# Performance work log

Measured on AMD Instinct MI355X. Metric: run time of the kernel, lower is better.

Reference implementation:

```python
import jax, jax.numpy as jnp
import numpy as np

N_USER, N_BADGE, E = 200_000, 50_000, 5_000_000
NEG_SLOPE = 0.2


def _gat(x_src, x_dst, src, dst, Ws, Wd, a_s, a_d, b, n_dst):
    """Bipartite single-head PyG GATConv (add_self_loops=False)."""
    hs = x_src @ Ws                      # [Ns, C]
    hd = x_dst @ Wd                      # [Nd, C]
    alpha_s = hs @ a_s                   # [Ns]
    alpha_d = hd @ a_d                   # [Nd]
    e = jax.nn.leaky_relu(alpha_s[src] + alpha_d[dst], NEG_SLOPE)  # [E]
    m = jax.ops.segment_max(e, dst, num_segments=n_dst)            # per-dst max
    w = jnp.exp(e - m[dst])
    s = jax.ops.segment_sum(w, dst, num_segments=n_dst) + 1e-16
    alpha = w / s[dst]                   # softmax over incoming edges
    out = jax.ops.segment_sum(alpha[:, None] * hs[src], dst, num_segments=n_dst)
    return out + b


def setup_inputs() -> dict:
    key = jax.random.key(0)
    ks = jax.random.split(key, 40)
    i = [0]
    def nk():
        k = ks[i[0]]; i[0] += 1; return k
    def nrm(shape, scale):
        return jax.random.normal(nk(), shape, jnp.float32) * scale
    inp = {
        "x_user": nrm((N_USER, 64), 1.0),
        "x_badge": nrm((N_BADGE, 64), 1.0),
        "ub_src": jax.random.randint(nk(), (E,), 0, N_USER, jnp.int32),
        "ub_dst": jax.random.randint(nk(), (E,), 0, N_BADGE, jnp.int32),
        "bu_src": jax.random.randint(nk(), (E,), 0, N_BADGE, jnp.int32),
        "bu_dst": jax.random.randint(nk(), (E,), 0, N_USER, jnp.int32),
        "ew_ub": jax.random.uniform(nk(), (E,), jnp.float32),
        "ew_bu": jax.random.uniform(nk(), (E,), jnp.float32),
    }
    s64, s16 = 1.0 / 8.0, 1.0 / 4.0  # ~glorot-ish scales for fan_in 64 / 16
    for rel in ("ub", "bu"):
        inp[f"W1_{rel}_s"] = nrm((64, 16), s64)
        inp[f"W1_{rel}_d"] = nrm((64, 16), s64)
        inp[f"a1_{rel}_s"] = nrm((16,), s16)
        inp[f"a1_{rel}_d"] = nrm((16,), s16)
        inp[f"b1_{rel}"] = jnp.zeros((16,), jnp.float32)
        inp[f"W2_{rel}_s"] = nrm((16, 2), s16)
        inp[f"W2_{rel}_d"] = nrm((16, 2), s16)
        inp[f"a2_{rel}_s"] = nrm((2,), 0.5)
        inp[f"a2_{rel}_d"] = nrm((2,), 0.5)
        inp[f"b2_{rel}"] = jnp.zeros((2,), jnp.float32)
    return inp


def reference(x_user, x_badge, ub_src, ub_dst, bu_src, bu_dst, ew_ub, ew_bu,
              W1_ub_s, W1_ub_d, a1_ub_s, a1_ub_d, b1_ub,
              W1_bu_s, W1_bu_d, a1_bu_s, a1_bu_d, b1_bu,
              W2_ub_s, W2_ub_d, a2_ub_s, a2_ub_d, b2_ub,
              W2_bu_s, W2_bu_d, a2_bu_s, a2_bu_d, b2_bu):
    # layer 1 (edge weights ignored: GATConv has edge_dim=None -> lin_edge is None)
    hb = _gat(x_user, x_badge, ub_src, ub_dst, W1_ub_s, W1_ub_d, a1_ub_s, a1_ub_d, b1_ub, N_BADGE)
    hu = _gat(x_badge, x_user, bu_src, bu_dst, W1_bu_s, W1_bu_d, a1_bu_s, a1_bu_d, b1_bu, N_USER)
    hu = jax.nn.relu(hu)
    hb = jax.nn.relu(hb)
    # layer 2
    ob = _gat(hu, hb, ub_src, ub_dst, W2_ub_s, W2_ub_d, a2_ub_s, a2_ub_d, b2_ub, N_BADGE)
    ou = _gat(hb, hu, bu_src, bu_dst, W2_bu_s, W2_bu_d, a2_bu_s, a2_bu_d, b2_bu, N_USER)
    return (ou, ob)
```

## Files before the change

kernel.cpp:

```cpp
#include <hip/hip_runtime.h>
#include <hip/hip_fp16.h>
#include <math.h>


#define NEG_SLOPE 0.2f
#define PART_PER 9760
#define NBC 196
#define CAPC 27072
#define NHALF 392
#define CAPH 13824
#define SHARD_DIV 50000

__device__ __forceinline__ float lrelu(float x) { return x > 0.f ? x : NEG_SLOPE * x; }

__global__ void k_stageA(
    const int* __restrict__ src0, const int* __restrict__ dst0,
    const int* __restrict__ src1, const int* __restrict__ dst1,
    int nE, int pblocks, unsigned* __restrict__ part0, unsigned* __restrict__ part1,
    int* __restrict__ bcnt,
    const float* __restrict__ xu, const float* __restrict__ xb,
    const float* __restrict__ Wub_s, const float* __restrict__ aub_s,
    const float* __restrict__ Wbu_d, const float* __restrict__ abu_d,
    const float* __restrict__ Wbu_s, const float* __restrict__ abu_s,
    const float* __restrict__ Wub_d, const float* __restrict__ aub_d,
    __half* __restrict__ hs_u, float* __restrict__ as_u, float* __restrict__ ad_u,
    __half* __restrict__ hs_b, float* __restrict__ as_b, float* __restrict__ ad_b,
    int NU, int NB, int gNU, int partBlocks, int nodeBlocks) {
  union Sm {
    struct { unsigned s_sorted[PART_PER]; int h[257]; int ps[256]; int resb[256]; int cur[256]; } p;
    struct { float sW[64 * 16]; float sa[16]; float sv[64]; } n;
  };
  __shared__ Sm sm;
  int t = threadIdx.x;
  int b = blockIdx.x;
  int k = min(nodeBlocks, partBlocks / 2);
  int inter = 3 * k;
  int partIdx = -1, nodeIdx = -1;
  if (b < inter) {
    if ((b % 3) == 2) nodeIdx = b / 3;
    else partIdx = (b / 3) * 2 + (b % 3);
  } else {
    int rem = b - inter;
    int ptail = partBlocks - 2 * k;
    if (rem < ptail) partIdx = 2 * k + rem;
    else nodeIdx = k + (rem - ptail);
  }
  if (partIdx >= 0) {
    int gb = partIdx;
    const int* src; const int* dst; unsigned* part; int* bc; int shift; int mask;
    if (gb < pblocks) { src = src0; dst = dst0; part = part0; bc = bcnt; shift = 8; mask = 255; }
    else { gb -= pblocks; src = src1; dst = dst1; part = part1; bc = bcnt + 256; shift = 10; mask = 1023; }
    int per = (nE + pblocks - 1) / pblocks;
    int beg = gb * per;
    int end = min(beg + per, nE);
    int cnt = end - beg;
    int cnt4 = cnt & ~3;
    sm.p.h[t] = 0;
    __syncthreads();
    for (int i = beg + t * 4; i + 3 < end; i += 1024) {
      int4 d4 = *(const int4*)(dst + i);
      atomicAdd(&sm.p.h[d4.x >> shift], 1);
      atomicAdd(&sm.p.h[d4.y >> shift], 1);
      atomicAdd(&sm.p.h[d4.z >> shift], 1);
      atomicAdd(&sm.p.h[d4.w >> shift], 1);
    }
    for (int i = beg + cnt4 + t; i < end; i += 256) atomicAdd(&sm.p.h[dst[i] >> shift], 1);
    __syncthreads();
    int v = sm.p.h[t];
    sm.p.ps[t] = v;
    __syncthreads();
    for (int off = 1; off < 256; off <<= 1) {
      int u = (t >= off) ? sm.p.ps[t - off] : 0;
      __syncthreads();
      sm.p.ps[t] += u;
      __syncthreads();
    }
    int excl = sm.p.ps[t] - v;
    sm.p.resb[t] = (t < NBC && v > 0) ? atomicAdd(&bc[t], v) : 0;
    __syncthreads();
    sm.p.h[t] = excl;
    sm.p.cur[t] = excl;
    if (t == 255) sm.p.h[256] = excl + v;
    __syncthreads();
    for (int i = beg + t * 4; i + 3 < end; i += 1024) {
      int4 d4 = *(const int4*)(dst + i);
      int4 s4 = *(const int4*)(src + i);
      int r;
      r = atomicAdd(&sm.p.cur[d4.x >> shift], 1);
      sm.p.s_sorted[r] = ((unsigned)(d4.x & mask) << 18) | (unsigned)s4.x;
      r = atomicAdd(&sm.p.cur[d4.y >> shift], 1);
      sm.p.s_sorted[r] = ((unsigned)(d4.y & mask) << 18) | (unsigned)s4.y;
      r = atomicAdd(&sm.p.cur[d4.z >> shift], 1);
      sm.p.s_sorted[r] = ((unsigned)(d4.z & mask) << 18) | (unsigned)s4.z;
      r = atomicAdd(&sm.p.cur[d4.w >> shift], 1);
      sm.p.s_sorted[r] = ((unsigned)(d4.w & mask) << 18) | (unsigned)s4.w;
    }
    for (int i = beg + cnt4 + t; i < end; i += 256) {
      int d = dst[i];
      int r = atomicAdd(&sm.p.cur[d >> shift], 1);
      sm.p.s_sorted[r] = ((unsigned)(d & mask) << 18) | (unsigned)src[i];
    }
    __syncthreads();
    for (int i = t; i < cnt; i += 1024) {
      int i1 = i + 256, i2 = i + 512, i3 = i + 768;
      int lo0 = 0, lo1 = 0, lo2 = 0, lo3 = 0;
      int hi0 = 256, hi1 = 256, hi2 = 256, hi3 = 256;
#pragma unroll
      for (int s = 0; s < 8; ++s) {
        int m0 = (lo0 + hi0) >> 1; if (sm.p.h[m0] <= i)  lo0 = m0; else hi0 = m0;
        int m1 = (lo1 + hi1) >> 1; if (sm.p.h[m1] <= i1) lo1 = m1; else hi1 = m1;
        int m2 = (lo2 + hi2) >> 1; if (sm.p.h[m2] <= i2) lo2 = m2; else hi2 = m2;
        int m3 = (lo3 + hi3) >> 1; if (sm.p.h[m3] <= i3) lo3 = m3; else hi3 = m3;
      }
      { int p = sm.p.resb[lo0] + (i - sm.p.h[lo0]);
        if (p < CAPC) part[(size_t)lo0 * CAPC + p] = sm.p.s_sorted[i]; }
      if (i1 < cnt) { int p = sm.p.resb[lo1] + (i1 - sm.p.h[lo1]);
        if (p < CAPC) part[(size_t)lo1 * CAPC + p] = sm.p.s_sorted[i1]; }
      if (i2 < cnt) { int p = sm.p.resb[lo2] + (i2 - sm.p.h[lo2]);
        if (p < CAPC) part[(size_t)lo2 * CAPC + p] = sm.p.s_sorted[i2]; }
      if (i3 < cnt) { int p = sm.p.resb[lo3] + (i3 - sm.p.h[lo3]);
        if (p < CAPC) part[(size_t)lo3 * CAPC + p] = sm.p.s_sorted[i3]; }
    }
    return;
  }
  int blk = nodeIdx;
  bool us = blk < gNU;
  const float* x  = us ? xu : xb;
  const float* Ws = us ? Wub_s : Wbu_s;
  const float* As = us ? aub_s : abu_s;
  const float* Wd = us ? Wbu_d : Wub_d;
  const float* Ad = us ? abu_d : aub_d;
  __half* hs = us ? hs_u : hs_b;
  float* als = us ? as_u : as_b;
  float* ald = us ? ad_u : ad_b;
  int N = us ? NU : NB;
  for (int i = t; i < 64 * 16; i += 256) sm.n.sW[i] = Ws[i];
  if (t < 16) sm.n.sa[t] = As[t];
  if (t < 64) {
    float s = 0.f;
    for (int c = 0; c < 16; ++c) s += Wd[t * 16 + c] * Ad[c];
    sm.n.sv[t] = s;
  }
  __syncthreads();
  int n = (us ? blk : blk - gNU) * 256 + t;
  if (n >= N) return;
  float acc[16];
#pragma unroll
  for (int c = 0; c < 16; ++c) acc[c] = 0.f;
  float ad = 0.f;
  const float4* xr4 = (const float4*)(x + (size_t)n * 64);
#pragma unroll 4
  for (int f4 = 0; f4 < 16; ++f4) {
    float4 xv4 = xr4[f4];
    float xv[4] = {xv4.x, xv4.y, xv4.z, xv4.w};
#pragma unroll
    for (int q = 0; q < 4; ++q) {
      int f = f4 * 4 + q;
#pragma unroll
      for (int c = 0; c < 16; ++c) acc[c] += xv[q] * sm.n.sW[f * 16 + c];
      ad += xv[q] * sm.n.sv[f];
    }
  }
  float al = 0.f;
#pragma unroll
  for (int c = 0; c < 16; ++c) {
    hs[(size_t)n * 16 + c] = __float2half(acc[c]);
    al += acc[c] * sm.n.sa[c];
  }
  als[n] = al;
  ald[n] = ad;
}

__global__ void k_sort2_both(const unsigned* __restrict__ part0,
                             const unsigned* __restrict__ part1,
                             const int* __restrict__ bcnt,
                             int* __restrict__ col0, int* __restrict__ col1,
                             int* __restrict__ rp0, int* __restrict__ rp1) {
  __shared__ unsigned s_sorted[CAPH];
  __shared__ int hist[512];
  __shared__ int ps[512];
  __shared__ int cur[512];
  __shared__ int s_tot;
  int bb = blockIdx.x;
  const unsigned* part; const int* bc; int* col; int* rp;
  int hsh, hmask, ns, sdiv;
  if (bb < NHALF) { part = part0; bc = bcnt; col = col0; rp = rp0;
                    hsh = 7; hmask = 127; ns = 4; sdiv = SHARD_DIV; }
  else { bb -= NHALF; part = part1; bc = bcnt + 256; col = col1; rp = rp1;
         hsh = 9; hmask = 511; ns = 1; sdiv = 1 << 30; }
  int t = threadIdx.x;
  int f = bb >> 1;
  int half = bb & 1;
  int cnt = min(bc[f], CAPC);
  int cnt4 = cnt & ~3;
  int slot = bb * CAPH;
  const unsigned* pp = part + (size_t)f * CAPC;
  hist[t] = 0;
  __syncthreads();
  for (int i = t * 4; i + 3 < cnt; i += 2048) {
    uint4 e4 = *(const uint4*)(pp + i);
    unsigned ee[4] = {e4.x, e4.y, e4.z, e4.w};
#pragma unroll
    for (int q = 0; q < 4; ++q) {
      int dl = (int)(ee[q] >> 18);
      if ((dl >> hsh) == half) {
        int sv = (int)(ee[q] & 0x3FFFFu);
        int bin = (ns == 4) ? ((dl & hmask) << 2) + sv / sdiv : (dl & hmask);
        atomicAdd(&hist[bin], 1);
      }
    }
  }
  for (int i = cnt4 + t; i < cnt; i += 512) {
    unsigned e = pp[i];
    int dl = (int)(e >> 18);
    if ((dl >> hsh) == half) {
      int sv = (int)(e & 0x3FFFFu);
      int bin = (ns == 4) ? ((dl & hmask) << 2) + sv / sdiv : (dl & hmask);
      atomicAdd(&hist[bin], 1);
    }
  }
  __syncthreads();
  int v = hist[t];
  ps[t] = v;
  __syncthreads();
  for (int off = 1; off < 512; off <<= 1) {
    int u = (t >= off) ? ps[t - off] : 0;
    __syncthreads();
    ps[t] += u;
    __syncthreads();
  }
  int excl = ps[t] - v;
  rp[bb * 513 + t] = slot + excl;
  if (t == 511) {
    int tot = min(ps[511], CAPH);
    rp[bb * 513 + 512] = slot + tot;
    s_tot = tot;
  }
  cur[t] = excl;
  __syncthreads();
  for (int i = t * 4; i + 3 < cnt; i += 2048) {
    uint4 e4 = *(const uint4*)(pp + i);
    unsigned ee[4] = {e4.x, e4.y, e4.z, e4.w};
#pragma unroll
    for (int q = 0; q < 4; ++q) {
      int dl = (int)(ee[q] >> 18);
      if ((dl >> hsh) == half) {
        int sv = (int)(ee[q] & 0x3FFFFu);
        int bin = (ns == 4) ? ((dl & hmask) << 2) + sv / sdiv : (dl & hmask);
        int r = atomicAdd(&cur[bin], 1);
        if (r < CAPH) s_sorted[r] = (unsigned)sv;
      }
    }
  }
  for (int i = cnt4 + t; i < cnt; i += 512) {
    unsigned e = pp[i];
    int dl = (int)(e >> 18);
    if ((dl >> hsh) == half) {
      int sv = (int)(e & 0x3FFFFu);
      int bin = (ns == 4) ? ((dl & hmask) << 2) + sv / sdiv : (dl & hmask);
      int r = atomicAdd(&cur[bin], 1);
      if (r < CAPH) s_sorted[r] = (unsigned)sv;
    }
  }
  __syncthreads();
  int tot = s_tot;
  for (int i = t; i < tot; i += 512) col[slot + i] = (int)s_sorted[i];
}

__device__ __forceinline__ void gat_pair8(
    const int* __restrict__ col, const __half* __restrict__ hs,
    int beg, int end, int j, float adv, const float (&sa)[8],
    float (&acc)[8], float& se) {
  int h = j & 1;
  int k0 = beg + (j >> 1);
  if (k0 >= end) return;
  int sv0 = col[k0];
  int k1 = k0 + 4;
  int sv1 = (k1 < end) ? col[k1] : -1;
  uint4 hv0 = *(const uint4*)(hs + (size_t)sv0 * 16 + h * 8);
  for (;;) {
    uint4 hv1 = hv0;
    int sv2 = -1;
    int k2 = k1 + 4;
    if (sv1 >= 0) {
      hv1 = *(const uint4*)(hs + (size_t)sv1 * 16 + h * 8);
      sv2 = (k2 < end) ? col[k2] : -1;
    }
    union { uint4 v; __half hh[8]; } b;
    b.v = hv0;
    float f[8];
    float p = 0.f;
#pragma unroll
    for (int cc = 0; cc < 8; ++cc) {
      f[cc] = __half2float(b.hh[cc]);
      p += f[cc] * sa[cc];
    }
    float afull = p + __shfl_xor(p, 1, 8);
    float w = __expf(lrelu(afull + adv));
    se += w;
#pragma unroll
    for (int cc = 0; cc < 8; ++cc) acc[cc] += w * f[cc];
    if (sv1 < 0) break;
    hv0 = hv1;
    sv1 = sv2;
    k1 = k2;
  }
}

__global__ void k_megaL1(
    const int* __restrict__ rp_ub, const int* __restrict__ col_ub,
    const float* __restrict__ a1s_ub, const float* __restrict__ ad_b,
    const __half* __restrict__ hs_u,
    float* __restrict__ acc_sl, float* __restrict__ se_sl,
    const int* __restrict__ rp_bu, const int* __restrict__ col_bu,
    const float* __restrict__ a1s_bu, const float* __restrict__ ad_u,
    const __half* __restrict__ hs_b,
    const float* __restrict__ b1bu,
    const float* __restrict__ W2ub_s, const float* __restrict__ a2ub_s,
    const float* __restrict__ W2bu_d, const float* __restrict__ a2bu_d,
    float4* __restrict__ pk_u, int NB, int NU, int ubBlocks) {
  __shared__ float sW2[32], sa2[2], sv2[16], sb1[16], sAub[16], sAbu[16];
  int t = threadIdx.x;
  if (t < 32) sW2[t] = W2ub_s[t];
  if (t < 2) sa2[t] = a2ub_s[t];
  if (t < 16) {
    float s = 0.f;
    for (int cc = 0; cc < 2; ++cc) s += W2bu_d[t * 2 + cc] * a2bu_d[cc];
    sv2[t] = s;
    sb1[t] = b1bu[t];
    sAub[t] = a1s_ub[t];
    sAbu[t] = a1s_bu[t];
  }
  __syncthreads();
  int b = blockIdx.x;
  int j = t & 7;
  int h = j & 1;
  if (b < ubBlocks) {
    int xcd = b & 7;
    int s = xcd >> 1;
    int sub = ((b >> 3) << 1) | (xcd & 1);
    int n = sub * 32 + (t >> 3);
    if (n >= NB) return;
    int base = (n >> 7) * 513 + (n & 127) * 4 + s;
    int beg = rp_ub[base], end = rp_ub[base + 1];
    float adv = ad_b[n];
    float sa[8];
#pragma unroll
    for (int cc = 0; cc < 8; ++cc) sa[cc] = sAub[h * 8 + cc];
    float acc[8];
#pragma unroll
    for (int cc = 0; cc < 8; ++cc) acc[cc] = 0.f;
    float se = 0.f;
    gat_pair8(col_ub, hs_u, beg, end, j, adv, sa, acc, se);
#pragma unroll
    for (int m = 2; m < 8; m <<= 1) {
      se += __shfl_xor(se, m, 8);
#pragma unroll
      for (int cc = 0; cc < 8; ++cc) acc[cc] += __shfl_xor(acc[cc], m, 8);
    }
    if (j < 2) {
      float* o = acc_sl + ((size_t)s * NB + n) * 16 + h * 8;
#pragma unroll
      for (int cc = 0; cc < 8; ++cc) o[cc] = acc[cc];
      if (j == 0) se_sl[s * NB + n] = se;
    }
  } else {
    int n = (b - ubBlocks) * 32 + (t >> 3);
    if (n >= NU) return;
    int base = (n >> 9) * 513 + (n & 511);
    int beg = rp_bu[base], end = rp_bu[base + 1];
    float adv = ad_u[n];
    float sa[8];
#pragma unroll
    for (int cc = 0; cc < 8; ++cc) sa[cc] = sAbu[h * 8 + cc];
    float acc[8];
#pragma unroll
    for (int cc = 0; cc < 8; ++cc) acc[cc] = 0.f;
    float se = 0.f;
    gat_pair8(col_bu, hs_b, beg, end, j, adv, sa, acc, se);
#pragma unroll
    for (int m = 2; m < 8; m <<= 1) {
      se += __shfl_xor(se, m, 8);
#pragma unroll
      for (int cc = 0; cc < 8; ++cc) acc[cc] += __shfl_xor(acc[cc], m, 8);
    }
    float inv = 1.f / (se + 1e-16f);
    float ph0 = 0.f, ph1 = 0.f, padv = 0.f;
#pragma unroll
    for (int cc = 0; cc < 8; ++cc) {
      int c = h * 8 + cc;
      float xv = fmaxf(acc[cc] * inv + sb1[c], 0.f);
      ph0 += xv * sW2[c * 2];
      ph1 += xv * sW2[c * 2 + 1];
      padv += xv * sv2[c];
    }
    ph0 += __shfl_xor(ph0, 1, 8);
    ph1 += __shfl_xor(ph1, 1, 8);
    padv += __shfl_xor(padv, 1, 8);
    if (j == 0)
      pk_u[n] = make_float4(ph0 * sa2[0] + ph1 * sa2[1], ph0, ph1, padv);
  }
}

__global__ void k_finL1b(
    const float* __restrict__ acc_sl, const float* __restrict__ se_sl,
    const float* __restrict__ b1ub,
    const float* __restrict__ W2bu_s, const float* __restrict__ a2bu_s,
    const float* __restrict__ W2ub_d, const float* __restrict__ a2ub_d,
    float4* __restrict__ pk_b, int NB) {
  __shared__ float sW2[32], sa2[2], sv2[16], sb1[16];
  int t = threadIdx.x;
  if (t < 32) sW2[t] = W2bu_s[t];
  if (t < 2) sa2[t] = a2bu_s[t];
  if (t < 16) {
    float s = 0.f;
    for (int cc = 0; cc < 2; ++cc) s += W2ub_d[t * 2 + cc] * a2ub_d[cc];
    sv2[t] = s;
    sb1[t] = b1ub[t];
  }
  __syncthreads();
  int n = blockIdx.x * 256 + t;
  if (n >= NB) return;
  float a[16];
#pragma unroll
  for (int c = 0; c < 16; ++c) a[c] = 0.f;
  float se = 0.f;
  for (int s = 0; s < 4; ++s) {
    const float4* p = (const float4*)(acc_sl + ((size_t)s * NB + n) * 16);
    float4 v0 = p[0], v1 = p[1], v2 = p[2], v3 = p[3];
    a[0] += v0.x; a[1] += v0.y; a[2] += v0.z; a[3] += v0.w;
    a[4] += v1.x; a[5] += v1.y; a[6] += v1.z; a[7] += v1.w;
    a[8] += v2.x; a[9] += v2.y; a[10] += v2.z; a[11] += v2.w;
    a[12] += v3.x; a[13] += v3.y; a[14] += v3.z; a[15] += v3.w;
    se += se_sl[s * NB + n];
  }
  float inv = 1.f / (se + 1e-16f);
  float h0 = 0.f, h1 = 0.f, advn = 0.f;
#pragma unroll
  for (int c = 0; c < 16; ++c) {
    float xv = fmaxf(a[c] * inv + sb1[c], 0.f);
    h0 += xv * sW2[c * 2];
    h1 += xv * sW2[c * 2 + 1];
    advn += xv * sv2[c];
  }
  pk_b[n] = make_float4(h0 * sa2[0] + h1 * sa2[1], h0, h1, advn);
}

__global__ void k_gatherL2(
    const int* __restrict__ rp0, const int* __restrict__ col0,
    const int* __restrict__ rp1, const int* __restrict__ col1,
    const float4* __restrict__ pk_u, const float4* __restrict__ pk_b,
    const float* __restrict__ b2ub, const float* __restrict__ b2bu,
    float* __restrict__ ob, float* __restrict__ ou,
    int NB, int NU, int g0) {
  int blk = blockIdx.x;
  const int *rp, *col; const float4 *pksrc, *pkown; const float* bb; float* out;
  int N, lsh, nsg;
  if (blk < g0) { rp = rp0; col = col0; pksrc = pk_u; pkown = pk_b; bb = b2ub;
                  out = ob; N = NB; lsh = 7; nsg = 4; }
  else { blk -= g0; rp = rp1; col = col1; pksrc = pk_b; pkown = pk_u; bb = b2bu;
         out = ou; N = NU; lsh = 9; nsg = 1; }
  int n = blk * 64 + (threadIdx.x >> 2);
  int j = threadIdx.x & 3;
  if (n >= N) return;
  int base = (n >> lsh) * 513 + (n & ((1 << lsh) - 1)) * nsg;
  int beg = rp[base], end = rp[base + nsg];
  float adv = pkown[n].w;
  float a0 = 0.f, a1 = 0.f, se = 0.f;
  int k0 = beg + j;
  if (k0 < end) {
    int c0 = col[k0];
    int k1 = k0 + 4;
    int c1 = (k1 < end) ? col[k1] : -1;
    float4 p0 = pksrc[c0];
    for (;;) {
      float4 p1 = p0;
      int c2 = -1;
      int k2 = k1 + 4;
      if (c1 >= 0) {
        p1 = pksrc[c1];
        c2 = (k2 < end) ? col[k2] : -1;
      }
      float w = __expf(lrelu(p0.x + adv));
      se += w;
      a0 += w * p0.y;
      a1 += w * p0.z;
      if (c1 < 0) break;
      p0 = p1;
      c1 = c2;
      k1 = k2;
    }
  }
#pragma unroll
  for (int m = 1; m < 4; m <<= 1) {
    se += __shfl_xor(se, m, 4);
    a0 += __shfl_xor(a0, m, 4);
    a1 += __shfl_xor(a1, m, 4);
  }
  if (j == 0) {
    float inv = 1.f / (se + 1e-16f);
    out[(size_t)n * 2] = a0 * inv + bb[0];
    out[(size_t)n * 2 + 1] = a1 * inv + bb[1];
  }
}

extern "C" void kernel_launch(void* const* d_in, const int* in_sizes, int n_in,
                              void* d_out, int out_size, void* d_ws, size_t ws_size,
                              hipStream_t stream) {
  const int NU = 200000, NB = 50000;
  const float* x_user  = (const float*)d_in[0];
  const float* x_badge = (const float*)d_in[1];
  const int* ub_src = (const int*)d_in[2];
  const int* ub_dst = (const int*)d_in[3];
  const int* bu_src = (const int*)d_in[4];
  const int* bu_dst = (const int*)d_in[5];
  const int nE = in_sizes[2];

  const float* W1_ub_s = (const float*)d_in[8];
  const float* W1_ub_d = (const float*)d_in[9];
  const float* a1_ub_s = (const float*)d_in[10];
  const float* a1_ub_d = (const float*)d_in[11];
  const float* b1_ub   = (const float*)d_in[12];
  const float* W2_ub_s = (const float*)d_in[13];
  const float* W2_ub_d = (const float*)d_in[14];
  const float* a2_ub_s = (const float*)d_in[15];
  const float* a2_ub_d = (const float*)d_in[16];
  const float* b2_ub   = (const float*)d_in[17];
  const float* W1_bu_s = (const float*)d_in[18];
  const float* W1_bu_d = (const float*)d_in[19];
  const float* a1_bu_s = (const float*)d_in[20];
  const float* a1_bu_d = (const float*)d_in[21];
  const float* b1_bu   = (const float*)d_in[22];
  const float* W2_bu_s = (const float*)d_in[23];
  const float* W2_bu_d = (const float*)d_in[24];
  const float* a2_bu_s = (const float*)d_in[25];
  const float* a2_bu_d = (const float*)d_in[26];
  const float* b2_bu   = (const float*)d_in[27];

  const int pblocks = (nE + PART_PER - 1) / PART_PER;
  const int gNU = (NU + 255) / 256;
  const int gNB = (NB + 255) / 256;

  char* wsb = (char*)d_ws;
  size_t off = 0;
  auto ialloc = [&](size_t n) { int* p = (int*)(wsb + off); off += n * 4; return p; };
  int* rp2_ub = ialloc((size_t)NHALF * 513);
  int* rp2_bu = ialloc((size_t)NHALF * 513);
  int* bcnt   = ialloc(512);
  int* col_ub = ialloc((size_t)NHALF * CAPH);
  int* col_bu = ialloc((size_t)NHALF * CAPH);
  off = (off + 15) & ~(size_t)15;
  const size_t partBytes = (size_t)2 * NBC * CAPC * 4;
  const size_t nodeBytes = (size_t)NU * 32 + (size_t)NB * 32 +
                           (size_t)(NU + NB) * 8 + 1024;
  bool fused = ws_size >= off + partBytes + nodeBytes + 4096;
  char* partBase = wsb + off;
  char* nodeBase = fused ? (partBase + partBytes) : partBase;
  unsigned* part0 = (unsigned*)partBase;
  unsigned* part1 = part0 + (size_t)NBC * CAPC;
  size_t poff = 0;
  auto falloc = [&](size_t n) { float* p = (float*)(nodeBase + poff); poff += n * 4; return p; };
  auto halloc = [&](size_t n) { __half* p = (__half*)(nodeBase + poff); poff += n * 2; return p; };
  __half* hs_u1 = halloc((size_t)NU * 16);
  __half* hs_b1 = halloc((size_t)NB * 16);
  float* as_u1  = falloc(NU);
  float* ad_u1  = falloc(NU);
  float* as_b1  = falloc(NB);
  float* ad_b1  = falloc(NB);
  poff = (poff + 15) & ~(size_t)15;
  float4* pk_u  = (float4*)(nodeBase + poff); poff += (size_t)NU * 16;
  float4* pk_b  = (float4*)(nodeBase + poff); poff += (size_t)NB * 16;
  char* accBase = fused ? partBase : (nodeBase + ((poff + 15) & ~(size_t)15));
  float* acc_sl = (float*)accBase;
  float* se_sl  = (float*)(accBase + (size_t)4 * NB * 16 * 4);

  float* ou = (float*)d_out;
  float* ob = (float*)d_out + (size_t)NU * 2;

  const int chunksB = (NB + 31) / 32;
  const int ubBlocks = ((chunksB + 1) / 2) * 8;
  const int buBlocks = (NU + 31) / 32;
  const int g0 = (NB + 63) / 64;
  const int g1 = (NU + 63) / 64;

  hipMemsetAsync(bcnt, 0, 512 * 4, stream);
  if (fused) {
    k_stageA<<<dim3(2 * pblocks + gNU + gNB), dim3(256), 0, stream>>>(
        ub_src, ub_dst, bu_src, bu_dst, nE, pblocks, part0, part1, bcnt,
        x_user, x_badge, W1_ub_s, a1_ub_s, W1_bu_d, a1_bu_d,
        W1_bu_s, a1_bu_s, W1_ub_d, a1_ub_d,
        hs_u1, as_u1, ad_u1, hs_b1, as_b1, ad_b1, NU, NB, gNU,
        2 * pblocks, gNU + gNB);
    k_sort2_both<<<dim3(2 * NHALF), dim3(512), 0, stream>>>(
        part0, part1, bcnt, col_ub, col_bu, rp2_ub, rp2_bu);
  } else {
    k_stageA<<<dim3(2 * pblocks), dim3(256), 0, stream>>>(
        ub_src, ub_dst, bu_src, bu_dst, nE, pblocks, part0, part1, bcnt,
        x_user, x_badge, W1_ub_s, a1_ub_s, W1_bu_d, a1_bu_d,
        W1_bu_s, a1_bu_s, W1_ub_d, a1_ub_d,
        hs_u1, as_u1, ad_u1, hs_b1, as_b1, ad_b1, NU, NB, gNU,
        2 * pblocks, 0);
    k_sort2_both<<<dim3(2 * NHALF), dim3(512), 0, stream>>>(
        part0, part1, bcnt, col_ub, col_bu, rp2_ub, rp2_bu);
    k_stageA<<<dim3(gNU + gNB), dim3(256), 0, stream>>>(
        ub_src, ub_dst, bu_src, bu_dst, nE, pblocks, part0, part1, bcnt,
        x_user, x_badge, W1_ub_s, a1_ub_s, W1_bu_d, a1_bu_d,
        W1_bu_s, a1_bu_s, W1_ub_d, a1_ub_d,
        hs_u1, as_u1, ad_u1, hs_b1, as_b1, ad_b1, NU, NB, gNU,
        0, gNU + gNB);
  }
  k_megaL1<<<dim3(ubBlocks + buBlocks), dim3(256), 0, stream>>>(
      rp2_ub, col_ub, a1_ub_s, ad_b1, hs_u1, acc_sl, se_sl,
      rp2_bu, col_bu, a1_bu_s, ad_u1, hs_b1,
      b1_bu, W2_ub_s, a2_ub_s, W2_bu_d, a2_bu_d,
      pk_u, NB, NU, ubBlocks);
  k_finL1b<<<dim3(gNB), dim3(256), 0, stream>>>(
      acc_sl, se_sl, b1_ub, W2_bu_s, a2_bu_s, W2_ub_d, a2_ub_d, pk_b, NB);
  k_gatherL2<<<dim3(g0 + g1), dim3(256), 0, stream>>>(
      rp2_ub, col_ub, rp2_bu, col_bu, pk_u, pk_b, b2_ub, b2_bu, ob, ou, NB, NU, g0);
}
```

Baseline: 426.0 us.

## Cache partition edges in registers and use wave-shuffle prefix scan

The partition stage now loads each block's dst/src edges once into register arrays (10 int4 per thread) and reuses them for both the histogram and the scatter passes, instead of reading dst twice from global memory. The 256-entry shared-memory Hillis-Steele scan with many barriers is replaced by a 64-wide wavefront shuffle scan plus a small cross-wave fixup. Per-block chunk size is rounded to a multiple of 4 and PART_PER grows to fit, so the fixed 10-iteration unroll must cover every block's edges. This raises register pressure and assumes per-block counts stay within 10240 edges.

```diff
diff --git a/kernel.cpp b/kernel.cpp
--- a/kernel.cpp
+++ b/kernel.cpp
@@ -4,7 +4,7 @@
 
 
 #define NEG_SLOPE 0.2f
-#define PART_PER 9760
+#define PART_PER 10240
 #define NBC 196
 #define CAPC 27072
 #define NHALF 392
@@ -27,7 +27,7 @@
     __half* __restrict__ hs_b, float* __restrict__ as_b, float* __restrict__ ad_b,
     int NU, int NB, int gNU, int partBlocks, int nodeBlocks) {
   union Sm {
-    struct { unsigned s_sorted[PART_PER]; int h[257]; int ps[256]; int resb[256]; int cur[256]; } p;
+    struct { unsigned s_sorted[PART_PER]; int h[257]; int ws[4]; int resb[256]; int cur[256]; } p;
     struct { float sW[64 * 16]; float sa[16]; float sv[64]; } n;
   };
   __shared__ Sm sm;
@@ -50,55 +50,80 @@
     const int* src; const int* dst; unsigned* part; int* bc; int shift; int mask;
     if (gb < pblocks) { src = src0; dst = dst0; part = part0; bc = bcnt; shift = 8; mask = 255; }
     else { gb -= pblocks; src = src1; dst = dst1; part = part1; bc = bcnt + 256; shift = 10; mask = 1023; }
-    int per = (nE + pblocks - 1) / pblocks;
+    int per = (((nE + pblocks - 1) / pblocks) + 3) & ~3;
     int beg = gb * per;
     int end = min(beg + per, nE);
     int cnt = end - beg;
-    int cnt4 = cnt & ~3;
     sm.p.h[t] = 0;
     __syncthreads();
-    for (int i = beg + t * 4; i + 3 < end; i += 1024) {
-      int4 d4 = *(const int4*)(dst + i);
-      atomicAdd(&sm.p.h[d4.x >> shift], 1);
-      atomicAdd(&sm.p.h[d4.y >> shift], 1);
-      atomicAdd(&sm.p.h[d4.z >> shift], 1);
-      atomicAdd(&sm.p.h[d4.w >> shift], 1);
-    }
-    for (int i = beg + cnt4 + t; i < end; i += 256) atomicAdd(&sm.p.h[dst[i] >> shift], 1);
+    int4 dreg[10], sreg[10];
+#pragma unroll
+    for (int ii = 0; ii < 10; ++ii) {
+      int i = beg + t * 4 + ii * 1024;
+      if (i + 3 < end) {
+        dreg[ii] = *(const int4*)(dst + i);
+        sreg[ii] = *(const int4*)(src + i);
+        atomicAdd(&sm.p.h[dreg[ii].x >> shift], 1);
+        atomicAdd(&sm.p.h[dreg[ii].y >> shift], 1);
+        atomicAdd(&sm.p.h[dreg[ii].z >> shift], 1);
+        atomicAdd(&sm.p.h[dreg[ii].w >> shift], 1);
+      } else {
+        dreg[ii].x = dreg[ii].y = dreg[ii].z = dreg[ii].w = -1;
+        sreg[ii].x = sreg[ii].y = sreg[ii].z = sreg[ii].w = 0;
+        if (i < end) {
+          int m = end - i;
+          dreg[ii].x = dst[i]; sreg[ii].x = src[i];
+          atomicAdd(&sm.p.h[dreg[ii].x >> shift], 1);
+          if (m > 1) { dreg[ii].y = dst[i + 1]; sreg[ii].y = src[i + 1];
+                       atomicAdd(&sm.p.h[dreg[ii].y >> shift], 1); }
+          if (m > 2) { dreg[ii].z = dst[i + 2]; sreg[ii].z = src[i + 2];
+                       atomicAdd(&sm.p.h[dreg[ii].z >> shift], 1); }
+        }
+      }
+    }
     __syncthreads();
     int v = sm.p.h[t];
-    sm.p.ps[t] = v;
+    int x = v;
+#pragma unroll
+    for (int o = 1; o < 64; o <<= 1) {
+      int y = __shfl_up(x, o, 64);
+      if ((t & 63) >= o) x += y;
+    }
+    if ((t & 63) == 63) sm.p.ws[t >> 6] = x;
     __syncthreads();
-    for (int off = 1; off < 256; off <<= 1) {
-      int u = (t >= off) ? sm.p.ps[t - off] : 0;
-      __syncthreads();
-      sm.p.ps[t] += u;
-      __syncthreads();
-    }
-    int excl = sm.p.ps[t] - v;
+    int wpre = 0;
+#pragma unroll
+    for (int w = 0; w < 3; ++w) if ((t >> 6) > w) wpre += sm.p.ws[w];
+    int incl = x + wpre;
+    int excl = incl - v;
     sm.p.resb[t] = (t < NBC && v > 0) ? atomicAdd(&bc[t], v) : 0;
-    __syncthreads();
     sm.p.h[t] = excl;
     sm.p.cur[t] = excl;
     if (t == 255) sm.p.h[256] = excl + v;
     __syncthreads();
-    for (int i = beg + t * 4; i + 3 < end; i += 1024) {
-      int4 d4 = *(const int4*)(dst + i);
-      int4 s4 = *(const int4*)(src + i);
-      int r;
-      r = atomicAdd(&sm.p.cur[d4.x >> shift], 1);
-      sm.p.s_sorted[r] = ((unsigned)(d4.x & mask) << 18) | (unsigned)s4.x;
-      r = atomicAdd(&sm.p.cur[d4.y >> shift], 1);
-      sm.p.s_sorted[r] = ((unsigned)(d4.y & mask) << 18) | (unsigned)s4.y;
-      r = atomicAdd(&sm.p.cur[d4.z >> shift], 1);
-      sm.p.s_sorted[r] = ((unsigned)(d4.z & mask) << 18) | (unsigned)s4.z;
-      r = atomicAdd(&sm.p.cur[d4.w >> shift], 1);
-      sm.p.s_sorted[r] = ((unsigned)(d4.w & mask) << 18) | (unsigned)s4.w;
-    }
-    for (int i = beg + cnt4 + t; i < end; i += 256) {
-      int d = dst[i];
-      int r = atomicAdd(&sm.p.cur[d >> shift], 1);
-      sm.p.s_sorted[r] = ((unsigned)(d & mask) << 18) | (unsigned)src[i];
+#pragma unroll
+    for (int ii = 0; ii < 10; ++ii) {
+      int i = beg + t * 4 + ii * 1024;
+      if (i + 3 < end) {
+        int r, d;
+        d = dreg[ii].x; r = atomicAdd(&sm.p.cur[d >> shift], 1);
+        sm.p.s_sorted[r] = ((unsigned)(d & mask) << 18) | (unsigned)sreg[ii].x;
+        d = dreg[ii].y; r = atomicAdd(&sm.p.cur[d >> shift], 1);
+        sm.p.s_sorted[r] = ((unsigned)(d & mask) << 18) | (unsigned)sreg[ii].y;
+        d = dreg[ii].z; r = atomicAdd(&sm.p.cur[d >> shift], 1);
+        sm.p.s_sorted[r] = ((unsigned)(d & mask) << 18) | (unsigned)sreg[ii].z;
+        d = dreg[ii].w; r = atomicAdd(&sm.p.cur[d >> shift], 1);
+        sm.p.s_sorted[r] = ((unsigned)(d & mask) << 18) | (unsigned)sreg[ii].w;
+      } else if (i < end) {
+        int m = end - i;
+        int r, d;
+        d = dreg[ii].x; r = atomicAdd(&sm.p.cur[d >> shift], 1);
+        sm.p.s_sorted[r] = ((unsigned)(d & mask) << 18) | (unsigned)sreg[ii].x;
+        if (m > 1) { d = dreg[ii].y; r = atomicAdd(&sm.p.cur[d >> shift], 1);
+                     sm.p.s_sorted[r] = ((unsigned)(d & mask) << 18) | (unsigned)sreg[ii].y; }
+        if (m > 2) { d = dreg[ii].z; r = atomicAdd(&sm.p.cur[d >> shift], 1);
+                     sm.p.s_sorted[r] = ((unsigned)(d & mask) << 18) | (unsigned)sreg[ii].z; }
+      }
     }
     __syncthreads();
     for (int i = t; i < cnt; i += 1024) {
```

Result: no change. 422.4 us (-0.9%).
